# Optimization experiments

Hardware: AMD Instinct MI355X
Metric: run time of the kernel (lower is better)

## Reference

```python
import jax, jax.numpy as jnp
import numpy as np

N_NODES = 100000
N_EDGES = 1600000
F_IN, F_HID, F_OUT = 128, 128, 16


def _add_self_loops(edge_index, n):
    loop = jnp.arange(n, dtype=edge_index.dtype)
    src = jnp.concatenate([edge_index[0], loop])
    dst = jnp.concatenate([edge_index[1], loop])
    return src, dst


def _gcn_conv(x, W, b, src, dst, n):
    # linear transform first (PyG/jraphx GCNConv order)
    h = x @ W  # [N, out]
    # symmetric normalization with unit edge weights, degrees on dst (incl. self loops)
    ones = jnp.ones(src.shape[0], dtype=h.dtype)
    deg = jax.ops.segment_sum(ones, dst, num_segments=n)
    dinv = jnp.where(deg > 0, jax.lax.rsqrt(deg), jnp.zeros((), h.dtype))
    norm = dinv[src] * dinv[dst]  # [E']
    msg = h[src] * norm[:, None]  # gather + scale: [E', out]
    out = jax.ops.segment_sum(msg, dst, num_segments=n)  # scatter-add
    return out + b


def setup_inputs() -> dict:
    key = jax.random.key(0)
    k1, k2, k3, k4, k5, k6 = jax.random.split(key, 6)
    x = jax.random.normal(k1, (N_NODES, F_IN), dtype=jnp.float32)
    edge_index = jax.random.randint(k2, (2, N_EDGES), 0, N_NODES, dtype=jnp.int32)
    W1 = jax.random.normal(k3, (F_IN, F_HID), dtype=jnp.float32) * (1.0 / np.sqrt(F_IN))
    b1 = jnp.zeros((F_HID,), dtype=jnp.float32)
    W2 = jax.random.normal(k4, (F_HID, F_OUT), dtype=jnp.float32) * (1.0 / np.sqrt(F_HID))
    b2 = jnp.zeros((F_OUT,), dtype=jnp.float32)
    return {"x": x, "edge_index": edge_index, "W1": W1, "b1": b1, "W2": W2, "b2": b2}


def reference(x, edge_index, W1, b1, W2, b2):
    n = x.shape[0]
    src, dst = _add_self_loops(edge_index, n)
    h = _gcn_conv(x, W1, b1, src, dst, n)
    h = jax.nn.relu(h)
    # dropout is identity in eval mode
    return _gcn_conv(h, W2, b2, src, dst, n)
```

## Files before the change

kernel.cpp:

```cpp
#include <hip/hip_runtime.h>
#include <hip/hip_fp16.h>

#define NN 100000
#define NE 1600000
#define ETOT (NE + NN)
#define FIN 128
#define FHID 128
#define FOUT 16

#define NB1 196
#define PBLK 256
#define PCH (NE / PBLK)
#define P2_CAP 10240

typedef _Float16 f16x8 __attribute__((ext_vector_type(8)));
typedef float f32x4 __attribute__((ext_vector_type(4)));


__global__ __launch_bounds__(256) void k_cnt(const int* __restrict__ dst,
                                             int* __restrict__ cnt) {
    __shared__ int h[NB1];
    int tid = threadIdx.x;
    for (int i = tid; i < NB1; i += 256) h[i] = 0;
    __syncthreads();
    int e0 = blockIdx.x * PCH;
    for (int e = e0 + tid; e < e0 + PCH; e += 256)
        atomicAdd(&h[dst[e] >> 9], 1);
    __syncthreads();
    for (int i = tid; i < NB1; i += 256) cnt[blockIdx.x * NB1 + i] = h[i];
}

__global__ __launch_bounds__(256) void k_offs(const int* __restrict__ cnt,
                                              int* __restrict__ woffp,
                                              int* __restrict__ bintot) {
    __shared__ int s[256];
    int b = blockIdx.x;
    int t = threadIdx.x;
    int v = cnt[t * NB1 + b];
    s[t] = v;
    __syncthreads();
    for (int off = 1; off < 256; off <<= 1) {
        int xv = (t >= off) ? s[t - off] : 0;
        __syncthreads();
        s[t] += xv;
        __syncthreads();
    }
    woffp[t * NB1 + b] = s[t] - v;
    if (t == 255) bintot[b] = s[255];
}

__global__ void k_bstart(const int* __restrict__ bintot,
                         int* __restrict__ binstart, int* __restrict__ rowptr) {
    __shared__ int s[256];
    int t = threadIdx.x;
    int v = (t < NB1) ? bintot[t] : 0;
    s[t] = v;
    __syncthreads();
    for (int off = 1; off < 256; off <<= 1) {
        int xv = (t >= off) ? s[t - off] : 0;
        __syncthreads();
        s[t] += xv;
        __syncthreads();
    }
    if (t < NB1) binstart[t] = s[t] - v;
    if (t == NB1 - 1) binstart[NB1] = s[t];
    if (t == 0) rowptr[NN] = ETOT;
}

__global__ __launch_bounds__(256) void k_scat(const int* __restrict__ ei,
                                              const int* __restrict__ woffp,
                                              const int* __restrict__ binstart,
                                              unsigned* __restrict__ binned) {
    __shared__ int cur[NB1];
    int tid = threadIdx.x;
    int k = blockIdx.x;
    for (int i = tid; i < NB1; i += 256) cur[i] = binstart[i] + woffp[k * NB1 + i];
    __syncthreads();
    int e0 = k * PCH;
    for (int e = e0 + tid; e < e0 + PCH; e += 256) {
        int s = ei[e], d = ei[NE + e];
        int b = d >> 9;
        int pos = atomicAdd(&cur[b], 1);
        binned[pos] = (unsigned)s | ((unsigned)(d & 511) << 17);
    }
}

__global__ __launch_bounds__(256) void k_build(const unsigned* __restrict__ binned,
                                               const int* __restrict__ binstart,
                                               int* __restrict__ rowptr,
                                               float* __restrict__ dinv,
                                               int* __restrict__ col) {
    __shared__ int dcnt[512];
    __shared__ int pref[512];
    __shared__ int sc[256];
    __shared__ int ord[P2_CAP];
    int b = blockIdx.x;
    int tid = threadIdx.x;
    int n0 = b * 512;
    int nn = min(512, NN - n0);
    int eb = binstart[b];
    int ecnt = binstart[b + 1] - eb;
    int colbase = eb + n0;
    dcnt[tid] = 0; dcnt[tid + 256] = 0;
    __syncthreads();
    for (int e = tid; e < ecnt; e += 256)
        atomicAdd(&dcnt[binned[eb + e] >> 17], 1);
    __syncthreads();
    int d0 = (2 * tid < nn)     ? dcnt[2 * tid] + 1     : 0;
    int d1 = (2 * tid + 1 < nn) ? dcnt[2 * tid + 1] + 1 : 0;
    sc[tid] = d0 + d1;
    __syncthreads();
    for (int off = 1; off < 256; off <<= 1) {
        int xv = (tid >= off) ? sc[tid - off] : 0;
        __syncthreads();
        sc[tid] += xv;
        __syncthreads();
    }
    int base = sc[tid] - d0 - d1;
    pref[2 * tid] = base;
    pref[2 * tid + 1] = base + d0;
    __syncthreads();
    for (int i = tid; i < nn; i += 256) {
        int p = pref[i];
        rowptr[n0 + i] = colbase + p;
        dinv[n0 + i] = rsqrtf((float)(dcnt[i] + 1));
        ord[p] = n0 + i;
    }
    __syncthreads();
    for (int i = tid; i < nn; i += 256) dcnt[i] = pref[i] + 1;
    __syncthreads();
    for (int e = tid; e < ecnt; e += 256) {
        unsigned p = binned[eb + e];
        int pos = atomicAdd(&dcnt[p >> 17], 1);
        int sv = (int)(p & 0x1FFFFu);
        if (pos < P2_CAP) ord[pos] = sv; else col[colbase + pos] = sv;
    }
    __syncthreads();
    int tot = ecnt + nn;
    int lim = min(tot, P2_CAP);
    for (int i = tid; i < lim; i += 256) col[colbase + i] = ord[i];
}


__global__ __launch_bounds__(256) void k_w1t(const float* __restrict__ W,
                                             _Float16* __restrict__ WT) {
    __shared__ _Float16 tl[16][136];
    int b = blockIdx.x;
    int tid = threadIdx.x;
    #pragma unroll
    for (int i = 0; i < 8; ++i) {
        int idx = tid + i * 256;
        int k = idx >> 7, n = idx & 127;
        tl[k][n] = (_Float16)W[(b * 16 + k) * FHID + n];
    }
    __syncthreads();
    #pragma unroll
    for (int i = 0; i < 8; ++i) {
        int idx = tid + i * 256;
        int n = idx >> 4, k = idx & 15;
        WT[n * FIN + b * 16 + k] = tl[k][n];
    }
}


__global__ __launch_bounds__(256) void k_gemm1(const float* __restrict__ x,
                                               const _Float16* __restrict__ WT,
                                               const float* __restrict__ dinv,
                                               _Float16* __restrict__ h) {
    __shared__ _Float16 xs[64 * 128];
    __shared__ _Float16 ws[128 * 128];
    int tid = threadIdx.x;
    int m0 = blockIdx.x * 64;
    #pragma unroll
    for (int i = 0; i < 4; ++i) {
        int u = tid + i * 256;
        int r = u >> 4;
        int k0 = (u & 15) * 8;
        int row = m0 + r;
        f16x8 v = {};
        if (row < NN) {
            float4 a = *(const float4*)&x[(size_t)row * FIN + k0];
            float4 b = *(const float4*)&x[(size_t)row * FIN + k0 + 4];
            v[0] = (_Float16)a.x; v[1] = (_Float16)a.y;
            v[2] = (_Float16)a.z; v[3] = (_Float16)a.w;
            v[4] = (_Float16)b.x; v[5] = (_Float16)b.y;
            v[6] = (_Float16)b.z; v[7] = (_Float16)b.w;
        }
        *(f16x8*)&xs[r * 128 + (k0 ^ ((r & 7) * 8))] = v;
    }
    #pragma unroll
    for (int i = 0; i < 8; ++i) {
        int u = tid + i * 256;
        int n = u >> 4;
        int k0 = (u & 15) * 8;
        f16x8 v = *(const f16x8*)&WT[n * FIN + k0];
        *(f16x8*)&ws[n * 128 + (k0 ^ ((n & 7) * 8))] = v;
    }
    __syncthreads();
    int wave = tid >> 6, lane = tid & 63;
    int lm = lane & 15, lg = lane >> 4;
    f32x4 acc[8];
    #pragma unroll
    for (int t = 0; t < 8; ++t) acc[t] = (f32x4){0.f, 0.f, 0.f, 0.f};
    int am = wave * 16 + lm;
    #pragma unroll
    for (int s = 0; s < 4; ++s) {
        int ka = s * 32 + lg * 8;
        f16x8 af = *(const f16x8*)&xs[am * 128 + (ka ^ ((am & 7) * 8))];
        #pragma unroll
        for (int t = 0; t < 8; ++t) {
            int bn = t * 16 + lm;
            f16x8 bf = *(const f16x8*)&ws[bn * 128 + (ka ^ ((bn & 7) * 8))];
            acc[t] = __builtin_amdgcn_mfma_f32_16x16x32_f16(af, bf, acc[t], 0, 0, 0);
        }
    }
    float dsc[4];
    #pragma unroll
    for (int r = 0; r < 4; ++r) {
        int grow = m0 + wave * 16 + lg * 4 + r;
        dsc[r] = (grow < NN) ? dinv[grow] : 0.f;
    }
    #pragma unroll
    for (int t = 0; t < 8; ++t) {
        int coln = t * 16 + lm;
        #pragma unroll
        for (int r = 0; r < 4; ++r) {
            int grow = m0 + wave * 16 + lg * 4 + r;
            if (grow < NN)
                h[(size_t)grow * FHID + coln] = (_Float16)(acc[t][r] * dsc[r]);
        }
    }
}


__device__ __forceinline__ void add_row8(float* acc, int4 raw) {
    const __half2* p = reinterpret_cast<const __half2*>(&raw);
    #pragma unroll
    for (int j = 0; j < 4; ++j) {
        float2 f = __half22float2(p[j]);
        acc[2 * j]     += f.x;
        acc[2 * j + 1] += f.y;
    }
}


__global__ __launch_bounds__(256) void k_agg1(const __half2* __restrict__ hf,
                                              const int* __restrict__ rowptr,
                                              const int* __restrict__ col,
                                              const float* __restrict__ dinv,
                                              const float* __restrict__ b1,
                                              __half2* __restrict__ out1) {
    int tid = threadIdx.x;
    int node = blockIdx.x * 16 + (tid >> 4);
    int lane = tid & 15;
    int beg = rowptr[node];
    int end = rowptr[node + 1];
    float acc[8] = {};
    int e = beg;
    for (; e + 4 <= end; e += 4) {
        int s0 = col[e], s1 = col[e + 1], s2 = col[e + 2], s3 = col[e + 3];
        int4 r0 = *reinterpret_cast<const int4*>(hf + (size_t)s0 * 64 + lane * 4);
        int4 r1 = *reinterpret_cast<const int4*>(hf + (size_t)s1 * 64 + lane * 4);
        int4 r2 = *reinterpret_cast<const int4*>(hf + (size_t)s2 * 64 + lane * 4);
        int4 r3 = *reinterpret_cast<const int4*>(hf + (size_t)s3 * 64 + lane * 4);
        add_row8(acc, r0);
        add_row8(acc, r1);
        add_row8(acc, r2);
        add_row8(acc, r3);
    }
    for (; e < end; ++e) {
        int s = col[e];
        int4 r = *reinterpret_cast<const int4*>(hf + (size_t)s * 64 + lane * 4);
        add_row8(acc, r);
    }
    float di = dinv[node];
    float4 bA = *(const float4*)&b1[lane * 8];
    float4 bB = *(const float4*)&b1[lane * 8 + 4];
    float o[8];
    o[0] = fmaxf(acc[0] * di + bA.x, 0.f);
    o[1] = fmaxf(acc[1] * di + bA.y, 0.f);
    o[2] = fmaxf(acc[2] * di + bA.z, 0.f);
    o[3] = fmaxf(acc[3] * di + bA.w, 0.f);
    o[4] = fmaxf(acc[4] * di + bB.x, 0.f);
    o[5] = fmaxf(acc[5] * di + bB.y, 0.f);
    o[6] = fmaxf(acc[6] * di + bB.z, 0.f);
    o[7] = fmaxf(acc[7] * di + bB.w, 0.f);
    __half2 ph[4];
    #pragma unroll
    for (int j = 0; j < 4; ++j) ph[j] = __floats2half2_rn(o[2 * j], o[2 * j + 1]);
    *reinterpret_cast<int4*>(out1 + (size_t)node * 64 + lane * 4) =
        *reinterpret_cast<int4*>(ph);
}


__global__ __launch_bounds__(256) void k_gemm2(const __half2* __restrict__ a,
                                               const float* __restrict__ W,
                                               const float* __restrict__ dinv,
                                               __half2* __restrict__ h2) {
    __shared__ __half2 xs[64][68];
    __shared__ float ws[FHID][FOUT];
    int tid = threadIdx.x;
    int m0 = blockIdx.x * 64;
    #pragma unroll
    for (int i = 0; i < 8; ++i) {
        int idx = tid + i * 256;
        ws[idx >> 4][idx & 15] = W[idx];
    }
    #pragma unroll
    for (int i = 0; i < 4; ++i) {
        int idx = tid + i * 256;
        int r = idx >> 4, q = idx & 15;
        int row = m0 + r;
        int4 v = make_int4(0, 0, 0, 0);
        if (row < NN) v = *reinterpret_cast<const int4*>(a + (size_t)row * 64 + q * 4);
        *reinterpret_cast<int4*>(&xs[r][q * 4]) = v;
    }
    __syncthreads();
    int cp = tid & 7, r = tid >> 3;
    float a00 = 0.f, a01 = 0.f, a10 = 0.f, a11 = 0.f;
    #pragma unroll 8
    for (int k2 = 0; k2 < 64; ++k2) {
        float2 f0 = __half22float2(xs[r][k2]);
        float2 f1 = __half22float2(xs[r + 32][k2]);
        float wa0 = ws[2 * k2][2 * cp],     wb0 = ws[2 * k2][2 * cp + 1];
        float wa1 = ws[2 * k2 + 1][2 * cp], wb1 = ws[2 * k2 + 1][2 * cp + 1];
        a00 += f0.x * wa0 + f0.y * wa1;
        a01 += f0.x * wb0 + f0.y * wb1;
        a10 += f1.x * wa0 + f1.y * wa1;
        a11 += f1.x * wb0 + f1.y * wb1;
    }
    int row0 = m0 + r, row1 = m0 + r + 32;
    if (row0 < NN) {
        float d = dinv[row0];
        h2[(size_t)row0 * 8 + cp] = __floats2half2_rn(a00 * d, a01 * d);
    }
    if (row1 < NN) {
        float d = dinv[row1];
        h2[(size_t)row1 * 8 + cp] = __floats2half2_rn(a10 * d, a11 * d);
    }
}


__global__ __launch_bounds__(256) void k_agg2(const __half2* __restrict__ h2,
                                              const int* __restrict__ rowptr,
                                              const int* __restrict__ col,
                                              const float* __restrict__ dinv,
                                              const float* __restrict__ b2,
                                              float* __restrict__ out) {
    int tid = threadIdx.x;
    int node = blockIdx.x * 128 + (tid >> 1);
    if (node >= NN) return;
    int l = tid & 1;
    int beg = rowptr[node];
    int end = rowptr[node + 1];
    float acc[8] = {};
    int e = beg;
    for (; e + 4 <= end; e += 4) {
        int s0 = col[e], s1 = col[e + 1], s2 = col[e + 2], s3 = col[e + 3];
        int4 r0 = *reinterpret_cast<const int4*>(h2 + (size_t)s0 * 8 + l * 4);
        int4 r1 = *reinterpret_cast<const int4*>(h2 + (size_t)s1 * 8 + l * 4);
        int4 r2 = *reinterpret_cast<const int4*>(h2 + (size_t)s2 * 8 + l * 4);
        int4 r3 = *reinterpret_cast<const int4*>(h2 + (size_t)s3 * 8 + l * 4);
        add_row8(acc, r0);
        add_row8(acc, r1);
        add_row8(acc, r2);
        add_row8(acc, r3);
    }
    for (; e < end; ++e) {
        int s = col[e];
        int4 r = *reinterpret_cast<const int4*>(h2 + (size_t)s * 8 + l * 4);
        add_row8(acc, r);
    }
    float di = dinv[node];
    float4 bA = *(const float4*)&b2[l * 8];
    float4 bB = *(const float4*)&b2[l * 8 + 4];
    float4 oA, oB;
    oA.x = acc[0] * di + bA.x;  oA.y = acc[1] * di + bA.y;
    oA.z = acc[2] * di + bA.z;  oA.w = acc[3] * di + bA.w;
    oB.x = acc[4] * di + bB.x;  oB.y = acc[5] * di + bB.y;
    oB.z = acc[6] * di + bB.z;  oB.w = acc[7] * di + bB.w;
    *(float4*)&out[(size_t)node * 16 + l * 8] = oA;
    *(float4*)&out[(size_t)node * 16 + l * 8 + 4] = oB;
}


extern "C" void kernel_launch(void* const* d_in, const int* in_sizes, int n_in,
                              void* d_out, int out_size, void* d_ws, size_t ws_size,
                              hipStream_t stream) {
    const float* x  = (const float*)d_in[0];
    const int*   ei = (const int*)d_in[1];
    const float* W1 = (const float*)d_in[2];
    const float* b1 = (const float*)d_in[3];
    const float* W2 = (const float*)d_in[4];
    const float* b2 = (const float*)d_in[5];
    float* out = (float*)d_out;

    char* ws = (char*)d_ws;
    size_t off = 0;
    #define WS_ALLOC(ptr_t, name, bytes) \
        ptr_t name = (ptr_t)(ws + off); off = (off + (size_t)(bytes) + 511) & ~(size_t)511;
    WS_ALLOC(int*,       rowptr,   ((size_t)NN + 1) * 4)
    WS_ALLOC(int*,       cnt,      (size_t)PBLK * NB1 * 4)
    WS_ALLOC(int*,       woffp,    (size_t)PBLK * NB1 * 4)
    WS_ALLOC(int*,       bintot,   (size_t)NB1 * 4)
    WS_ALLOC(int*,       binstart, ((size_t)NB1 + 1) * 4)
    WS_ALLOC(int*,       colv,     (size_t)ETOT * 4)
    WS_ALLOC(float*,     dinv,     (size_t)NN * 4)
    WS_ALLOC(_Float16*,  w1t,      (size_t)FIN * FHID * 2)
    WS_ALLOC(_Float16*,  hf,       (size_t)NN * FHID * 2)
    WS_ALLOC(__half2*,   out1f,    (size_t)NN * FHID * 2)
    WS_ALLOC(__half2*,   h2f,      (size_t)NN * FOUT * 2)
    #undef WS_ALLOC
    (void)ws_size; (void)in_sizes; (void)n_in; (void)out_size;

    unsigned* binned = (unsigned*)hf;

    k_cnt<<<PBLK, 256, 0, stream>>>(ei + NE, cnt);
    k_offs<<<NB1, 256, 0, stream>>>(cnt, woffp, bintot);
    k_bstart<<<1, 256, 0, stream>>>(bintot, binstart, rowptr);
    k_scat<<<PBLK, 256, 0, stream>>>(ei, woffp, binstart, binned);
    k_build<<<NB1, 256, 0, stream>>>(binned, binstart, rowptr, dinv, colv);

    k_w1t<<<8, 256, 0, stream>>>(W1, w1t);
    k_gemm1<<<(NN + 63) / 64, 256, 0, stream>>>(x, w1t, dinv, hf);
    k_agg1<<<NN / 16, 256, 0, stream>>>((const __half2*)hf, rowptr, colv, dinv, b1, out1f);

    k_gemm2<<<(NN + 63) / 64, 256, 0, stream>>>(out1f, W2, dinv, h2f);
    k_agg2<<<(NN + 127) / 128, 256, 0, stream>>>(h2f, rowptr, colv, dinv, b2, out);
}
```

Measured before the change: 174.9 us.

## Merge CSR build kernels into one cooperative kernel with grid syncs

Replaces the five graph-preprocessing kernels and the W1 transpose kernel with a single cooperative kernel of 256 blocks that separates the phases with grid.sync(). The W1 transpose runs alongside the bin-start scan in otherwise idle blocks. The goal is to remove launch overhead and the gaps between the small back-to-back kernels. In exchange, every block now holds the large ord shared array for all phases, which may limit occupancy, and cooperative launch requires all 256 blocks to be resident at once.

After: 303.5 us. +73.5%, slower.

```diff
diff --git a/kernel.cpp b/kernel.cpp
--- a/kernel.cpp
+++ b/kernel.cpp
@@ -1,5 +1,8 @@
 #include <hip/hip_runtime.h>
 #include <hip/hip_fp16.h>
+#include <hip/hip_cooperative_groups.h>
+
+namespace cg = cooperative_groups;
 
 #define NN 100000
 #define NE 1600000
@@ -17,148 +20,143 @@
 typedef float f32x4 __attribute__((ext_vector_type(4)));
 
 
-__global__ __launch_bounds__(256) void k_cnt(const int* __restrict__ dst,
-                                             int* __restrict__ cnt) {
-    __shared__ int h[NB1];
-    int tid = threadIdx.x;
-    for (int i = tid; i < NB1; i += 256) h[i] = 0;
-    __syncthreads();
-    int e0 = blockIdx.x * PCH;
-    for (int e = e0 + tid; e < e0 + PCH; e += 256)
-        atomicAdd(&h[dst[e] >> 9], 1);
-    __syncthreads();
-    for (int i = tid; i < NB1; i += 256) cnt[blockIdx.x * NB1 + i] = h[i];
-}
-
-__global__ __launch_bounds__(256) void k_offs(const int* __restrict__ cnt,
-                                              int* __restrict__ woffp,
-                                              int* __restrict__ bintot) {
-    __shared__ int s[256];
-    int b = blockIdx.x;
-    int t = threadIdx.x;
-    int v = cnt[t * NB1 + b];
-    s[t] = v;
-    __syncthreads();
-    for (int off = 1; off < 256; off <<= 1) {
-        int xv = (t >= off) ? s[t - off] : 0;
-        __syncthreads();
-        s[t] += xv;
-        __syncthreads();
-    }
-    woffp[t * NB1 + b] = s[t] - v;
-    if (t == 255) bintot[b] = s[255];
-}
-
-__global__ void k_bstart(const int* __restrict__ bintot,
-                         int* __restrict__ binstart, int* __restrict__ rowptr) {
-    __shared__ int s[256];
-    int t = threadIdx.x;
-    int v = (t < NB1) ? bintot[t] : 0;
-    s[t] = v;
-    __syncthreads();
-    for (int off = 1; off < 256; off <<= 1) {
-        int xv = (t >= off) ? s[t - off] : 0;
-        __syncthreads();
-        s[t] += xv;
-        __syncthreads();
-    }
-    if (t < NB1) binstart[t] = s[t] - v;
-    if (t == NB1 - 1) binstart[NB1] = s[t];
-    if (t == 0) rowptr[NN] = ETOT;
-}
-
-__global__ __launch_bounds__(256) void k_scat(const int* __restrict__ ei,
-                                              const int* __restrict__ woffp,
-                                              const int* __restrict__ binstart,
-                                              unsigned* __restrict__ binned) {
-    __shared__ int cur[NB1];
-    int tid = threadIdx.x;
-    int k = blockIdx.x;
-    for (int i = tid; i < NB1; i += 256) cur[i] = binstart[i] + woffp[k * NB1 + i];
-    __syncthreads();
-    int e0 = k * PCH;
-    for (int e = e0 + tid; e < e0 + PCH; e += 256) {
-        int s = ei[e], d = ei[NE + e];
-        int b = d >> 9;
-        int pos = atomicAdd(&cur[b], 1);
-        binned[pos] = (unsigned)s | ((unsigned)(d & 511) << 17);
-    }
-}
-
-__global__ __launch_bounds__(256) void k_build(const unsigned* __restrict__ binned,
-                                               const int* __restrict__ binstart,
-                                               int* __restrict__ rowptr,
-                                               float* __restrict__ dinv,
-                                               int* __restrict__ col) {
+__global__ __launch_bounds__(256) void k_buildall(const int* __restrict__ ei,
+                                                  const float* __restrict__ W1,
+                                                  int* __restrict__ cnt,
+                                                  int* __restrict__ woffp,
+                                                  int* __restrict__ bintot,
+                                                  int* __restrict__ binstart,
+                                                  int* __restrict__ rowptr,
+                                                  float* __restrict__ dinv,
+                                                  unsigned* __restrict__ binned,
+                                                  int* __restrict__ col,
+                                                  _Float16* __restrict__ WT) {
+    cg::grid_group grid = cg::this_grid();
     __shared__ int dcnt[512];
     __shared__ int pref[512];
     __shared__ int sc[256];
     __shared__ int ord[P2_CAP];
-    int b = blockIdx.x;
     int tid = threadIdx.x;
-    int n0 = b * 512;
-    int nn = min(512, NN - n0);
-    int eb = binstart[b];
-    int ecnt = binstart[b + 1] - eb;
-    int colbase = eb + n0;
-    dcnt[tid] = 0; dcnt[tid + 256] = 0;
-    __syncthreads();
-    for (int e = tid; e < ecnt; e += 256)
-        atomicAdd(&dcnt[binned[eb + e] >> 17], 1);
-    __syncthreads();
-    int d0 = (2 * tid < nn)     ? dcnt[2 * tid] + 1     : 0;
-    int d1 = (2 * tid + 1 < nn) ? dcnt[2 * tid + 1] + 1 : 0;
-    sc[tid] = d0 + d1;
-    __syncthreads();
-    for (int off = 1; off < 256; off <<= 1) {
-        int xv = (tid >= off) ? sc[tid - off] : 0;
-        __syncthreads();
-        sc[tid] += xv;
-        __syncthreads();
-    }
-    int base = sc[tid] - d0 - d1;
-    pref[2 * tid] = base;
-    pref[2 * tid + 1] = base + d0;
-    __syncthreads();
-    for (int i = tid; i < nn; i += 256) {
-        int p = pref[i];
-        rowptr[n0 + i] = colbase + p;
-        dinv[n0 + i] = rsqrtf((float)(dcnt[i] + 1));
-        ord[p] = n0 + i;
-    }
-    __syncthreads();
-    for (int i = tid; i < nn; i += 256) dcnt[i] = pref[i] + 1;
-    __syncthreads();
-    for (int e = tid; e < ecnt; e += 256) {
-        unsigned p = binned[eb + e];
-        int pos = atomicAdd(&dcnt[p >> 17], 1);
-        int sv = (int)(p & 0x1FFFFu);
-        if (pos < P2_CAP) ord[pos] = sv; else col[colbase + pos] = sv;
-    }
-    __syncthreads();
-    int tot = ecnt + nn;
-    int lim = min(tot, P2_CAP);
-    for (int i = tid; i < lim; i += 256) col[colbase + i] = ord[i];
-}
-
-
-__global__ __launch_bounds__(256) void k_w1t(const float* __restrict__ W,
-                                             _Float16* __restrict__ WT) {
-    __shared__ _Float16 tl[16][136];
-    int b = blockIdx.x;
-    int tid = threadIdx.x;
-    #pragma unroll
-    for (int i = 0; i < 8; ++i) {
-        int idx = tid + i * 256;
-        int k = idx >> 7, n = idx & 127;
-        tl[k][n] = (_Float16)W[(b * 16 + k) * FHID + n];
-    }
-    __syncthreads();
-    #pragma unroll
-    for (int i = 0; i < 8; ++i) {
-        int idx = tid + i * 256;
-        int n = idx >> 4, k = idx & 15;
-        WT[n * FIN + b * 16 + k] = tl[k][n];
+    int blk = blockIdx.x;
+    const int* dst = ei + NE;
+    int e0 = blk * PCH;
+
+    {
+        int* h = dcnt;
+        for (int i = tid; i < NB1; i += 256) h[i] = 0;
+        __syncthreads();
+        for (int e = e0 + tid; e < e0 + PCH; e += 256)
+            atomicAdd(&h[dst[e] >> 9], 1);
+        __syncthreads();
+        for (int i = tid; i < NB1; i += 256) cnt[blk * NB1 + i] = h[i];
+    }
+    grid.sync();
+
+    if (blk < NB1) {
+        int v = cnt[tid * NB1 + blk];
+        sc[tid] = v;
+        __syncthreads();
+        for (int off = 1; off < 256; off <<= 1) {
+            int xv = (tid >= off) ? sc[tid - off] : 0;
+            __syncthreads();
+            sc[tid] += xv;
+            __syncthreads();
+        }
+        woffp[tid * NB1 + blk] = sc[tid] - v;
+        if (tid == 255) bintot[blk] = sc[255];
+    }
+    grid.sync();
+
+    if (blk == 0) {
+        int v = (tid < NB1) ? bintot[tid] : 0;
+        sc[tid] = v;
+        __syncthreads();
+        for (int off = 1; off < 256; off <<= 1) {
+            int xv = (tid >= off) ? sc[tid - off] : 0;
+            __syncthreads();
+            sc[tid] += xv;
+            __syncthreads();
+        }
+        if (tid < NB1) binstart[tid] = sc[tid] - v;
+        if (tid == NB1 - 1) binstart[NB1] = sc[tid];
+        if (tid == 0) rowptr[NN] = ETOT;
+    } else if (blk <= 8) {
+        _Float16* tl = (_Float16*)ord;
+        int b = blk - 1;
+        #pragma unroll
+        for (int i = 0; i < 8; ++i) {
+            int idx = tid + i * 256;
+            int k = idx >> 7, n = idx & 127;
+            tl[k * 136 + n] = (_Float16)W1[(b * 16 + k) * FHID + n];
+        }
+        __syncthreads();
+        #pragma unroll
+        for (int i = 0; i < 8; ++i) {
+            int idx = tid + i * 256;
+            int n = idx >> 4, k = idx & 15;
+            WT[n * FIN + b * 16 + k] = tl[k * 136 + n];
+        }
+    }
+    grid.sync();
+
+    {
+        int* cur = dcnt;
+        for (int i = tid; i < NB1; i += 256)
+            cur[i] = binstart[i] + woffp[blk * NB1 + i];
+        __syncthreads();
+        for (int e = e0 + tid; e < e0 + PCH; e += 256) {
+            int s = ei[e], d = dst[e];
+            int b = d >> 9;
+            int pos = atomicAdd(&cur[b], 1);
+            binned[pos] = (unsigned)s | ((unsigned)(d & 511) << 17);
+        }
+    }
+    grid.sync();
+
+    if (blk < NB1) {
+        int n0 = blk * 512;
+        int nn = min(512, NN - n0);
+        int eb = binstart[blk];
+        int ecnt = binstart[blk + 1] - eb;
+        int colbase = eb + n0;
+        dcnt[tid] = 0; dcnt[tid + 256] = 0;
+        __syncthreads();
+        for (int e = tid; e < ecnt; e += 256)
+            atomicAdd(&dcnt[binned[eb + e] >> 17], 1);
+        __syncthreads();
+        int d0 = (2 * tid < nn)     ? dcnt[2 * tid] + 1     : 0;
+        int d1 = (2 * tid + 1 < nn) ? dcnt[2 * tid + 1] + 1 : 0;
+        sc[tid] = d0 + d1;
+        __syncthreads();
+        for (int off = 1; off < 256; off <<= 1) {
+            int xv = (tid >= off) ? sc[tid - off] : 0;
+            __syncthreads();
+            sc[tid] += xv;
+            __syncthreads();
+        }
+        int base = sc[tid] - d0 - d1;
+        pref[2 * tid] = base;
+        pref[2 * tid + 1] = base + d0;
+        __syncthreads();
+        for (int i = tid; i < nn; i += 256) {
+            int p = pref[i];
+            rowptr[n0 + i] = colbase + p;
+            dinv[n0 + i] = rsqrtf((float)(dcnt[i] + 1));
+            ord[p] = n0 + i;
+        }
+        __syncthreads();
+        for (int i = tid; i < nn; i += 256) dcnt[i] = pref[i] + 1;
+        __syncthreads();
+        for (int e = tid; e < ecnt; e += 256) {
+            unsigned p = binned[eb + e];
+            int pos = atomicAdd(&dcnt[p >> 17], 1);
+            int sv = (int)(p & 0x1FFFFu);
+            if (pos < P2_CAP) ord[pos] = sv; else col[colbase + pos] = sv;
+        }
+        __syncthreads();
+        int tot = ecnt + nn;
+        int lim = min(tot, P2_CAP);
+        for (int i = tid; i < lim; i += 256) col[colbase + i] = ord[i];
     }
 }
 
@@ -409,19 +407,20 @@
     WS_ALLOC(_Float16*,  w1t,      (size_t)FIN * FHID * 2)
     WS_ALLOC(_Float16*,  hf,       (size_t)NN * FHID * 2)
     WS_ALLOC(__half2*,   out1f,    (size_t)NN * FHID * 2)
-    WS_ALLOC(__half2*,   h2f,      (size_t)NN * FOUT * 2)
+    WS_ALLOC(__half2*,   h2f,     (size_t)NN * FOUT * 2)
     #undef WS_ALLOC
     (void)ws_size; (void)in_sizes; (void)n_in; (void)out_size;
 
     unsigned* binned = (unsigned*)hf;
 
-    k_cnt<<<PBLK, 256, 0, stream>>>(ei + NE, cnt);
-    k_offs<<<NB1, 256, 0, stream>>>(cnt, woffp, bintot);
-    k_bstart<<<1, 256, 0, stream>>>(bintot, binstart, rowptr);
-    k_scat<<<PBLK, 256, 0, stream>>>(ei, woffp, binstart, binned);
-    k_build<<<NB1, 256, 0, stream>>>(binned, binstart, rowptr, dinv, colv);
-
-    k_w1t<<<8, 256, 0, stream>>>(W1, w1t);
+    {
+        void* args[] = {(void*)&ei, (void*)&W1, (void*)&cnt, (void*)&woffp,
+                        (void*)&bintot, (void*)&binstart, (void*)&rowptr,
+                        (void*)&dinv, (void*)&binned, (void*)&colv, (void*)&w1t};
+        hipLaunchCooperativeKernel((const void*)k_buildall, dim3(PBLK), dim3(256),
+                                   args, 0, stream);
+    }
+
     k_gemm1<<<(NN + 63) / 64, 256, 0, stream>>>(x, w1t, dinv, hf);
     k_agg1<<<NN / 16, 256, 0, stream>>>((const __half2*)hf, rowptr, colv, dinv, b1, out1f);
 
```

## Merge preprocessing launches and move second GEMM onto MFMA

Applied to the files above, without the earlier changes.

Folds the W1 transpose into the edge-count kernel as extra blocks and removes the single-block bin-start scan by recomputing the prefix sum of bin totals inside the scatter and build kernels. This cuts the launch count from ten to eight. The second GEMM (128->16) is rewritten to use 16x16x32 f16 MFMA instructions with W2 staged transposed in shared memory, replacing the scalar FMA loop. Each block now repeats a small redundant scan, and W2 is rounded to fp16.

Result: faster. 167.6 us (median of 2 runs) (-4.2%).

```diff
diff --git a/kernel.cpp b/kernel.cpp
--- a/kernel.cpp
+++ b/kernel.cpp
@@ -17,22 +17,44 @@
 typedef float f32x4 __attribute__((ext_vector_type(4)));
 
 
-__global__ __launch_bounds__(256) void k_cnt(const int* __restrict__ dst,
-                                             int* __restrict__ cnt) {
-    __shared__ int h[NB1];
-    int tid = threadIdx.x;
-    for (int i = tid; i < NB1; i += 256) h[i] = 0;
-    __syncthreads();
-    int e0 = blockIdx.x * PCH;
-    for (int e = e0 + tid; e < e0 + PCH; e += 256)
-        atomicAdd(&h[dst[e] >> 9], 1);
-    __syncthreads();
-    for (int i = tid; i < NB1; i += 256) cnt[blockIdx.x * NB1 + i] = h[i];
+__global__ __launch_bounds__(256) void k_cnt(const int* __restrict__ ei,
+                                             const float* __restrict__ W1,
+                                             int* __restrict__ cnt,
+                                             _Float16* __restrict__ WT) {
+    int tid = threadIdx.x, blk = blockIdx.x;
+    if (blk < PBLK) {
+        __shared__ int h[NB1];
+        for (int i = tid; i < NB1; i += 256) h[i] = 0;
+        __syncthreads();
+        const int* dst = ei + NE;
+        int e0 = blk * PCH;
+        for (int e = e0 + tid; e < e0 + PCH; e += 256)
+            atomicAdd(&h[dst[e] >> 9], 1);
+        __syncthreads();
+        for (int i = tid; i < NB1; i += 256) cnt[blk * NB1 + i] = h[i];
+    } else {
+        __shared__ _Float16 tl[16][136];
+        int b = blk - PBLK;
+        #pragma unroll
+        for (int i = 0; i < 8; ++i) {
+            int idx = tid + i * 256;
+            int k = idx >> 7, n = idx & 127;
+            tl[k][n] = (_Float16)W1[(b * 16 + k) * FHID + n];
+        }
+        __syncthreads();
+        #pragma unroll
+        for (int i = 0; i < 8; ++i) {
+            int idx = tid + i * 256;
+            int n = idx >> 4, k = idx & 15;
+            WT[n * FIN + b * 16 + k] = tl[k][n];
+        }
+    }
 }
 
 __global__ __launch_bounds__(256) void k_offs(const int* __restrict__ cnt,
                                               int* __restrict__ woffp,
-                                              int* __restrict__ bintot) {
+                                              int* __restrict__ bintot,
+                                              int* __restrict__ rowptr) {
     __shared__ int s[256];
     int b = blockIdx.x;
     int t = threadIdx.x;
@@ -47,34 +69,27 @@
     }
     woffp[t * NB1 + b] = s[t] - v;
     if (t == 255) bintot[b] = s[255];
-}
-
-__global__ void k_bstart(const int* __restrict__ bintot,
-                         int* __restrict__ binstart, int* __restrict__ rowptr) {
-    __shared__ int s[256];
-    int t = threadIdx.x;
-    int v = (t < NB1) ? bintot[t] : 0;
-    s[t] = v;
-    __syncthreads();
-    for (int off = 1; off < 256; off <<= 1) {
-        int xv = (t >= off) ? s[t - off] : 0;
-        __syncthreads();
-        s[t] += xv;
-        __syncthreads();
-    }
-    if (t < NB1) binstart[t] = s[t] - v;
-    if (t == NB1 - 1) binstart[NB1] = s[t];
-    if (t == 0) rowptr[NN] = ETOT;
+    if (b == 0 && t == 0) rowptr[NN] = ETOT;
 }
 
 __global__ __launch_bounds__(256) void k_scat(const int* __restrict__ ei,
                                               const int* __restrict__ woffp,
-                                              const int* __restrict__ binstart,
+                                              const int* __restrict__ bintot,
                                               unsigned* __restrict__ binned) {
+    __shared__ int sc[256];
     __shared__ int cur[NB1];
     int tid = threadIdx.x;
     int k = blockIdx.x;
-    for (int i = tid; i < NB1; i += 256) cur[i] = binstart[i] + woffp[k * NB1 + i];
+    int v = (tid < NB1) ? bintot[tid] : 0;
+    sc[tid] = v;
+    __syncthreads();
+    for (int off = 1; off < 256; off <<= 1) {
+        int xv = (tid >= off) ? sc[tid - off] : 0;
+        __syncthreads();
+        sc[tid] += xv;
+        __syncthreads();
+    }
+    if (tid < NB1) cur[tid] = (sc[tid] - v) + woffp[k * NB1 + tid];
     __syncthreads();
     int e0 = k * PCH;
     for (int e = e0 + tid; e < e0 + PCH; e += 256) {
@@ -86,7 +101,7 @@
 }
 
 __global__ __launch_bounds__(256) void k_build(const unsigned* __restrict__ binned,
-                                               const int* __restrict__ binstart,
+                                               const int* __restrict__ bintot,
                                                int* __restrict__ rowptr,
                                                float* __restrict__ dinv,
                                                int* __restrict__ col) {
@@ -94,12 +109,22 @@
     __shared__ int pref[512];
     __shared__ int sc[256];
     __shared__ int ord[P2_CAP];
-    int b = blockIdx.x;
-    int tid = threadIdx.x;
-    int n0 = b * 512;
+    int blk = blockIdx.x;
+    int tid = threadIdx.x;
+    int bv = (tid < NB1) ? bintot[tid] : 0;
+    sc[tid] = bv;
+    __syncthreads();
+    for (int off = 1; off < 256; off <<= 1) {
+        int xv = (tid >= off) ? sc[tid - off] : 0;
+        __syncthreads();
+        sc[tid] += xv;
+        __syncthreads();
+    }
+    int ecnt = bintot[blk];
+    int eb = sc[blk] - ecnt;
+    __syncthreads();
+    int n0 = blk * 512;
     int nn = min(512, NN - n0);
-    int eb = binstart[b];
-    int ecnt = binstart[b + 1] - eb;
     int colbase = eb + n0;
     dcnt[tid] = 0; dcnt[tid + 256] = 0;
     __syncthreads();
@@ -139,27 +164,6 @@
     int tot = ecnt + nn;
     int lim = min(tot, P2_CAP);
     for (int i = tid; i < lim; i += 256) col[colbase + i] = ord[i];
-}
-
-
-__global__ __launch_bounds__(256) void k_w1t(const float* __restrict__ W,
-                                             _Float16* __restrict__ WT) {
-    __shared__ _Float16 tl[16][136];
-    int b = blockIdx.x;
-    int tid = threadIdx.x;
-    #pragma unroll
-    for (int i = 0; i < 8; ++i) {
-        int idx = tid + i * 256;
-        int k = idx >> 7, n = idx & 127;
-        tl[k][n] = (_Float16)W[(b * 16 + k) * FHID + n];
-    }
-    __syncthreads();
-    #pragma unroll
-    for (int i = 0; i < 8; ++i) {
-        int idx = tid + i * 256;
-        int n = idx >> 4, k = idx & 15;
-        WT[n * FIN + b * 16 + k] = tl[k][n];
-    }
 }
 
 
@@ -293,50 +297,43 @@
 }
 
 
-__global__ __launch_bounds__(256) void k_gemm2(const __half2* __restrict__ a,
+__global__ __launch_bounds__(256) void k_gemm2(const _Float16* __restrict__ a,
                                                const float* __restrict__ W,
                                                const float* __restrict__ dinv,
-                                               __half2* __restrict__ h2) {
-    __shared__ __half2 xs[64][68];
-    __shared__ float ws[FHID][FOUT];
-    int tid = threadIdx.x;
-    int m0 = blockIdx.x * 64;
+                                               _Float16* __restrict__ h2) {
+    __shared__ _Float16 w2t[16][136];
+    int tid = threadIdx.x;
     #pragma unroll
     for (int i = 0; i < 8; ++i) {
         int idx = tid + i * 256;
-        ws[idx >> 4][idx & 15] = W[idx];
-    }
-    #pragma unroll
-    for (int i = 0; i < 4; ++i) {
-        int idx = tid + i * 256;
-        int r = idx >> 4, q = idx & 15;
-        int row = m0 + r;
-        int4 v = make_int4(0, 0, 0, 0);
-        if (row < NN) v = *reinterpret_cast<const int4*>(a + (size_t)row * 64 + q * 4);
-        *reinterpret_cast<int4*>(&xs[r][q * 4]) = v;
-    }
-    __syncthreads();
-    int cp = tid & 7, r = tid >> 3;
-    float a00 = 0.f, a01 = 0.f, a10 = 0.f, a11 = 0.f;
-    #pragma unroll 8
-    for (int k2 = 0; k2 < 64; ++k2) {
-        float2 f0 = __half22float2(xs[r][k2]);
-        float2 f1 = __half22float2(xs[r + 32][k2]);
-        float wa0 = ws[2 * k2][2 * cp],     wb0 = ws[2 * k2][2 * cp + 1];
-        float wa1 = ws[2 * k2 + 1][2 * cp], wb1 = ws[2 * k2 + 1][2 * cp + 1];
-        a00 += f0.x * wa0 + f0.y * wa1;
-        a01 += f0.x * wb0 + f0.y * wb1;
-        a10 += f1.x * wa0 + f1.y * wa1;
-        a11 += f1.x * wb0 + f1.y * wb1;
-    }
-    int row0 = m0 + r, row1 = m0 + r + 32;
-    if (row0 < NN) {
-        float d = dinv[row0];
-        h2[(size_t)row0 * 8 + cp] = __floats2half2_rn(a00 * d, a01 * d);
-    }
-    if (row1 < NN) {
-        float d = dinv[row1];
-        h2[(size_t)row1 * 8 + cp] = __floats2half2_rn(a10 * d, a11 * d);
+        w2t[idx & 15][idx >> 4] = (_Float16)W[idx];
+    }
+    __syncthreads();
+    int wave = tid >> 6, lane = tid & 63;
+    int lm = lane & 15, lg = lane >> 4;
+    f16x8 bf[4];
+    #pragma unroll
+    for (int s = 0; s < 4; ++s)
+        bf[s] = *(const f16x8*)&w2t[lm][s * 32 + lg * 8];
+    int row0 = blockIdx.x * 256 + wave * 64;
+    #pragma unroll
+    for (int rt = 0; rt < 4; ++rt) {
+        int rbase = row0 + rt * 16;
+        f32x4 acc = {0.f, 0.f, 0.f, 0.f};
+        #pragma unroll
+        for (int s = 0; s < 4; ++s) {
+            int arow = rbase + lm;
+            f16x8 af = {};
+            if (arow < NN)
+                af = *(const f16x8*)&a[(size_t)arow * FHID + s * 32 + lg * 8];
+            acc = __builtin_amdgcn_mfma_f32_16x16x32_f16(af, bf[s], acc, 0, 0, 0);
+        }
+        #pragma unroll
+        for (int r = 0; r < 4; ++r) {
+            int row = rbase + lg * 4 + r;
+            if (row < NN)
+                h2[(size_t)row * FOUT + lm] = (_Float16)(acc[r] * dinv[row]);
+        }
     }
 }
 
@@ -403,28 +400,25 @@
     WS_ALLOC(int*,       cnt,      (size_t)PBLK * NB1 * 4)
     WS_ALLOC(int*,       woffp,    (size_t)PBLK * NB1 * 4)
     WS_ALLOC(int*,       bintot,   (size_t)NB1 * 4)
-    WS_ALLOC(int*,       binstart, ((size_t)NB1 + 1) * 4)
     WS_ALLOC(int*,       colv,     (size_t)ETOT * 4)
     WS_ALLOC(float*,     dinv,     (size_t)NN * 4)
     WS_ALLOC(_Float16*,  w1t,      (size_t)FIN * FHID * 2)
     WS_ALLOC(_Float16*,  hf,       (size_t)NN * FHID * 2)
     WS_ALLOC(__half2*,   out1f,    (size_t)NN * FHID * 2)
-    WS_ALLOC(__half2*,   h2f,      (size_t)NN * FOUT * 2)
+    WS_ALLOC(_Float16*,  h2f,      (size_t)NN * FOUT * 2)
     #undef WS_ALLOC
     (void)ws_size; (void)in_sizes; (void)n_in; (void)out_size;
 
     unsigned* binned = (unsigned*)hf;
 
-    k_cnt<<<PBLK, 256, 0, stream>>>(ei + NE, cnt);
-    k_offs<<<NB1, 256, 0, stream>>>(cnt, woffp, bintot);
-    k_bstart<<<1, 256, 0, stream>>>(bintot, binstart, rowptr);
-    k_scat<<<PBLK, 256, 0, stream>>>(ei, woffp, binstart, binned);
-    k_build<<<NB1, 256, 0, stream>>>(binned, binstart, rowptr, dinv, colv);
-
-    k_w1t<<<8, 256, 0, stream>>>(W1, w1t);
+    k_cnt<<<PBLK + 8, 256, 0, stream>>>(ei, W1, cnt, w1t);
+    k_offs<<<NB1, 256, 0, stream>>>(cnt, woffp, bintot, rowptr);
+    k_scat<<<PBLK, 256, 0, stream>>>(ei, woffp, bintot, binned);
+    k_build<<<NB1, 256, 0, stream>>>(binned, bintot, rowptr, dinv, colv);
+
     k_gemm1<<<(NN + 63) / 64, 256, 0, stream>>>(x, w1t, dinv, hf);
     k_agg1<<<NN / 16, 256, 0, stream>>>((const __half2*)hf, rowptr, colv, dinv, b1, out1f);
 
-    k_gemm2<<<(NN + 63) / 64, 256, 0, stream>>>(out1f, W2, dinv, h2f);
-    k_agg2<<<(NN + 127) / 128, 256, 0, stream>>>(h2f, rowptr, colv, dinv, b2, out);
-}
+    k_gemm2<<<(NN + 255) / 256, 256, 0, stream>>>((const _Float16*)out1f, W2, dinv, h2f);
+    k_agg2<<<(NN + 127) / 128, 256, 0, stream>>>((const __half2*)h2f, rowptr, colv, dinv, b2, out);
+}
```
